# Kernel tuning notes

Measured on AMD Instinct MI355X. Metric: run time of the kernel, lower is better.

Reference implementation:

```python
import jax, jax.numpy as jnp
import numpy as np

B, T, D, E, H, K = 4, 1024, 1024, 8, 4096, 2
N = B * T
EPS_LN = 1e-5
EPS_W = 1e-8
BAL_W = 0.01


def setup_inputs() -> dict:
    key = jax.random.key(0)
    ks = jax.random.split(key, 5)
    sc = 0.02
    return {
        "x": jax.random.normal(ks[0], (B, T, D), jnp.float32),
        "ln_gamma": jnp.ones((D,), jnp.float32),
        "ln_beta": jnp.zeros((D,), jnp.float32),
        "gate_w": jax.random.normal(ks[1], (D, E), jnp.float32) * sc,
        "w1": jax.random.normal(ks[2], (E, D, H), jnp.float32) * sc,
        "b1": jnp.zeros((E, H), jnp.float32),
        "w2": jax.random.normal(ks[3], (E, H, D), jnp.float32) * sc,
        "b2": jnp.zeros((E, D), jnp.float32),
    }


def reference(x, ln_gamma, ln_beta, gate_w, w1, b1, w2, b2):
    # LayerNorm (pre-norm), residual kept on raw x
    mu = jnp.mean(x, axis=-1, keepdims=True)
    var = jnp.var(x, axis=-1, keepdims=True)
    xn = (x - mu) * jax.lax.rsqrt(var + EPS_LN) * ln_gamma + ln_beta

    xf = xn.reshape(N, D)

    # Router (oscillator_state=None path): token gate only, k = top_k
    logits = xf @ gate_w                         # (N, E)
    router_probs = jax.nn.softmax(logits, axis=-1)
    top_w, top_i = jax.lax.top_k(router_probs, K)  # (N, K)
    top_w = top_w / (jnp.sum(top_w, axis=-1, keepdims=True) + EPS_W)

    # Dense per-token gate matrix: gates[n, e] = sum of top-k weights routed to e
    gates = jnp.zeros((N, E), xf.dtype).at[jnp.arange(N)[:, None], top_i].add(top_w)

    # Per-expert FFN (computed densely for all tokens, combined by sparse gates)
    h = jax.nn.gelu(jnp.einsum("nd,edh->enh", xf, w1) + b1[:, None, :], approximate=False)
    expert_out = jnp.einsum("enh,ehd->end", h, w2) + b2[:, None, :]  # (E, N, D)
    moe = jnp.einsum("ne,end->nd", gates, expert_out)

    output = x + moe.reshape(B, T, D)

    # Load-balance auxiliary loss
    counts = jnp.zeros((E,), xf.dtype).at[top_i.reshape(-1)].add(1.0)
    fraction = counts / N
    balance_loss = BAL_W * E * jnp.sum(fraction * jnp.mean(router_probs, axis=0))

    return output, balance_loss, router_probs
```

## Files before the change

kernel.cpp:

```cpp
#include <hip/hip_runtime.h>
#include <hip/hip_bf16.h>
#include <math.h>

#define DI   1024
#define EI   8
#define HI   4096
#define NI   4096

typedef __bf16 bf16x8 __attribute__((ext_vector_type(8)));
typedef float  f32x4  __attribute__((ext_vector_type(4)));

__device__ __forceinline__ unsigned short f2bf(float f) {
  union { float f; unsigned u; } c; c.f = f;
  unsigned r = c.u + 0x7FFF + ((c.u >> 16) & 1);
  return (unsigned short)(r >> 16);
}

__device__ __forceinline__ void async16(const void* g, void* l) {
  __builtin_amdgcn_global_load_lds(
      (const __attribute__((address_space(1))) void*)g,
      (__attribute__((address_space(3))) void*)l, 16, 0, 0);
}

__global__ __launch_bounds__(256) void ln_router_k(
    const float* __restrict__ x, const float* __restrict__ gamma,
    const float* __restrict__ beta, const float* __restrict__ gw,
    unsigned short* __restrict__ xnbf, float* __restrict__ probs_out,
    int* __restrict__ pairs, float2* __restrict__ gates2)
{
  const int t = threadIdx.x, lane = t & 63, wid = t >> 6;
  const int n = blockIdx.x * 4 + wid;

  const float4* xr = (const float4*)(x + (size_t)n * DI);
  float4 v[4];
  #pragma unroll
  for (int j = 0; j < 4; j++) v[j] = xr[lane * 4 + j];

  float s = 0.f, q = 0.f;
  #pragma unroll
  for (int j = 0; j < 4; j++) {
    s += v[j].x + v[j].y + v[j].z + v[j].w;
    q += v[j].x * v[j].x + v[j].y * v[j].y + v[j].z * v[j].z + v[j].w * v[j].w;
  }
  #pragma unroll
  for (int off = 1; off < 64; off <<= 1) {
    s += __shfl_xor(s, off);
    q += __shfl_xor(q, off);
  }
  const float mu = s * (1.0f / DI);
  const float rs = rsqrtf(q * (1.0f / DI) - mu * mu + 1e-5f);

  const float4* gr = (const float4*)gamma;
  const float4* br = (const float4*)beta;
  float xl[16];
  #pragma unroll
  for (int j = 0; j < 4; j++) {
    const float4 g4 = gr[lane * 4 + j];
    const float4 b4 = br[lane * 4 + j];
    xl[4 * j + 0] = (v[j].x - mu) * rs * g4.x + b4.x;
    xl[4 * j + 1] = (v[j].y - mu) * rs * g4.y + b4.y;
    xl[4 * j + 2] = (v[j].z - mu) * rs * g4.z + b4.z;
    xl[4 * j + 3] = (v[j].w - mu) * rs * g4.w + b4.w;
  }
  unsigned u[8];
  #pragma unroll
  for (int j = 0; j < 8; j++)
    u[j] = (unsigned)f2bf(xl[2 * j]) | ((unsigned)f2bf(xl[2 * j + 1]) << 16);
  uint4* dst = (uint4*)(xnbf + (size_t)n * DI + lane * 16);
  uint4 d0; d0.x = u[0]; d0.y = u[1]; d0.z = u[2]; d0.w = u[3];
  uint4 d1; d1.x = u[4]; d1.y = u[5]; d1.z = u[6]; d1.w = u[7];
  dst[0] = d0; dst[1] = d1;

  float p[8];
  #pragma unroll
  for (int e = 0; e < 8; e++) p[e] = 0.f;
  #pragma unroll
  for (int j = 0; j < 16; j++) {
    const float4* grow = (const float4*)(gw + (size_t)(lane * 16 + j) * EI);
    const float4 ga = grow[0], gb = grow[1];
    const float xv = xl[j];
    p[0] += xv * ga.x; p[1] += xv * ga.y; p[2] += xv * ga.z; p[3] += xv * ga.w;
    p[4] += xv * gb.x; p[5] += xv * gb.y; p[6] += xv * gb.z; p[7] += xv * gb.w;
  }
  #pragma unroll
  for (int e = 0; e < 8; e++)
    #pragma unroll
    for (int off = 1; off < 64; off <<= 1) p[e] += __shfl_xor(p[e], off);

  if (lane == 0) {
    float pm = -1e30f;
    #pragma unroll
    for (int e = 0; e < 8; e++) pm = fmaxf(pm, p[e]);
    float pr[8], ps = 0.f;
    #pragma unroll
    for (int e = 0; e < 8; e++) { pr[e] = expf(p[e] - pm); ps += pr[e]; }
    const float inv = 1.0f / ps;
    #pragma unroll
    for (int e = 0; e < 8; e++) {
      pr[e] *= inv;
      probs_out[(size_t)n * EI + e] = pr[e];
    }
    int i0 = 0; float m0 = pr[0];
    #pragma unroll
    for (int e = 1; e < 8; e++) if (pr[e] > m0) { m0 = pr[e]; i0 = e; }
    int i1 = -1; float m1 = -1e30f;
    #pragma unroll
    for (int e = 0; e < 8; e++) if (e != i0 && pr[e] > m1) { m1 = pr[e]; i1 = e; }
    const float ssum = m0 + m1 + 1e-8f;
    pairs[n] = i0 | (i1 << 8);
    float2 g2; g2.x = m0 / ssum; g2.y = m1 / ssum;
    gates2[n] = g2;
  }
}

__global__ __launch_bounds__(1024) void build_lists_k(
    const int* __restrict__ pairs, const float2* __restrict__ gates2,
    const float* __restrict__ probs, int* __restrict__ counts,
    int* __restrict__ offs, int* __restrict__ tok_list,
    float* __restrict__ gate_list, int2* __restrict__ ipos,
    float* __restrict__ out_bal)
{
  __shared__ int cnt[8];
  __shared__ int cur[8];
  __shared__ float wps[16][8];
  __shared__ float ps[8];
  const int t = threadIdx.x, lane = t & 63, wid = t >> 6;
  if (t < 8) cnt[t] = 0;
  __syncthreads();

  float acc[8];
  #pragma unroll
  for (int e = 0; e < 8; e++) acc[e] = 0.f;
  for (int n = t; n < NI; n += 1024) {
    const int pr = pairs[n];
    atomicAdd(&cnt[pr & 255], 1);
    atomicAdd(&cnt[pr >> 8], 1);
    const float4* prow = (const float4*)(probs + (size_t)n * EI);
    const float4 a = prow[0], b = prow[1];
    acc[0] += a.x; acc[1] += a.y; acc[2] += a.z; acc[3] += a.w;
    acc[4] += b.x; acc[5] += b.y; acc[6] += b.z; acc[7] += b.w;
  }
  #pragma unroll
  for (int e = 0; e < 8; e++)
    #pragma unroll
    for (int off = 1; off < 64; off <<= 1) acc[e] += __shfl_xor(acc[e], off);
  if (lane == 0)
    #pragma unroll
    for (int e = 0; e < 8; e++) wps[wid][e] = acc[e];
  __syncthreads();
  if (t < 8) {
    float sm = 0.f;
    for (int w = 0; w < 16; w++) sm += wps[w][t];
    ps[t] = sm;
  }
  __syncthreads();
  if (t == 0) {
    int off = 0; float bl = 0.f;
    for (int e = 0; e < 8; e++) {
      offs[e] = off; cur[e] = off; counts[e] = cnt[e];
      bl += (float)cnt[e] * ps[e];
      off += cnt[e];
    }
    *out_bal = 0.01f * 8.0f * bl / ((float)NI * (float)NI);
  }
  __syncthreads();
  for (int n = t; n < NI; n += 1024) {
    const int pr = pairs[n];
    const float2 g = gates2[n];
    const int p0 = atomicAdd(&cur[pr & 255], 1);
    tok_list[p0] = n; gate_list[p0] = g.x;
    const int p1 = atomicAdd(&cur[pr >> 8], 1);
    tok_list[p1] = n; gate_list[p1] = g.y;
    int2 ip; ip.x = p0; ip.y = p1;
    ipos[n] = ip;
  }
}

__global__ __launch_bounds__(256) void transpose_cvt_k(
    const float* __restrict__ in, unsigned short* __restrict__ out, int R, int C)
{
  __shared__ float tile[64][65];
  const size_t eoff = (size_t)blockIdx.z * (size_t)R * (size_t)C;
  const int c0 = blockIdx.x * 64, r0 = blockIdx.y * 64;
  const int t = threadIdx.x;
  {
    const int col = (t & 15) * 4;
    #pragma unroll
    for (int ii = 0; ii < 4; ii++) {
      const int row = (t >> 4) + ii * 16;
      const float4 v = *(const float4*)(in + eoff + (size_t)(r0 + row) * C + c0 + col);
      tile[row][col + 0] = v.x; tile[row][col + 1] = v.y;
      tile[row][col + 2] = v.z; tile[row][col + 3] = v.w;
    }
  }
  __syncthreads();
  {
    const int grp = t & 7;
    #pragma unroll
    for (int jj = 0; jj < 2; jj++) {
      const int orow = (t >> 3) + jj * 32;
      unsigned short vs[8];
      #pragma unroll
      for (int u = 0; u < 8; u++) vs[u] = f2bf(tile[grp * 8 + u][orow]);
      uint4 pk;
      pk.x = (unsigned)vs[0] | ((unsigned)vs[1] << 16);
      pk.y = (unsigned)vs[2] | ((unsigned)vs[3] << 16);
      pk.z = (unsigned)vs[4] | ((unsigned)vs[5] << 16);
      pk.w = (unsigned)vs[6] | ((unsigned)vs[7] << 16);
      *(uint4*)(out + eoff + (size_t)(c0 + orow) * R + r0 + grp * 8) = pk;
    }
  }
}

__global__ __launch_bounds__(256) void copy_x_k(const float* __restrict__ x, float* __restrict__ out)
{
  const size_t i = (size_t)blockIdx.x * 256 + threadIdx.x;
  ((float4*)out)[i] = ((const float4*)x)[i];
}

__global__ __launch_bounds__(256) void ffn1_k(
    const unsigned short* __restrict__ xnbf, const unsigned short* __restrict__ w1t,
    const float* __restrict__ b1, unsigned short* __restrict__ hbuf,
    const int* __restrict__ tok_list, const int* __restrict__ counts,
    const int* __restrict__ offsets)
{
  const int e = blockIdx.z;
  const int cnt = counts[e];
  const int mt = blockIdx.y;
  if (mt * 128 >= cnt) return;
  const int n0 = blockIdx.x * 128;
  const int t = threadIdx.x, lane = t & 63, w = t >> 6;
  const int wm = w & 1, wn = w >> 1;
  __shared__ __align__(16) unsigned short As[128 * 64];
  __shared__ __align__(16) unsigned short Bs[128 * 64];

  const int sub = lane >> 3;
  const int kc = (((lane & 7) ^ sub) * 8);
  const int eoff = offsets[e];
  const unsigned short* baseA[4];
  const unsigned short* baseB[4];
  #pragma unroll
  for (int r = 0; r < 4; r++) {
    int row = (w << 5) + r * 8 + sub;
    int idx = mt * 128 + row; if (idx > cnt - 1) idx = cnt - 1;
    int tok = tok_list[eoff + idx];
    baseA[r] = xnbf + (size_t)tok * DI + kc;
    baseB[r] = w1t + (size_t)e * HI * DI + (size_t)(n0 + row) * DI + kc;
  }

  f32x4 acc[4][4];
  const f32x4 zz = {0.f, 0.f, 0.f, 0.f};
  #pragma unroll
  for (int i = 0; i < 4; i++)
    #pragma unroll
    for (int j = 0; j < 4; j++) acc[i][j] = zz;

  const int mrow = (wm << 6) + (lane & 15);
  const int nrow = (wn << 6) + (lane & 15);
  const int ksw[2] = { (((lane >> 4) ^ (lane & 7)) * 8),
                       ((((lane >> 4) + 4) ^ (lane & 7)) * 8) };

  for (int k0 = 0; k0 < DI; k0 += 64) {
    __syncthreads();
    #pragma unroll
    for (int r = 0; r < 4; r++) {
      async16(baseA[r] + k0, &As[((w << 5) + r * 8) * 64]);
      async16(baseB[r] + k0, &Bs[((w << 5) + r * 8) * 64]);
    }
    __syncthreads();
    #pragma unroll
    for (int kk = 0; kk < 2; kk++) {
      const int ko = ksw[kk];
      bf16x8 af[4], bfr[4];
      #pragma unroll
      for (int mi = 0; mi < 4; mi++)
        af[mi] = *(const bf16x8*)&As[(mrow + mi * 16) * 64 + ko];
      #pragma unroll
      for (int ni = 0; ni < 4; ni++)
        bfr[ni] = *(const bf16x8*)&Bs[(nrow + ni * 16) * 64 + ko];
      #pragma unroll
      for (int mi = 0; mi < 4; mi++)
        #pragma unroll
        for (int ni = 0; ni < 4; ni++)
          acc[mi][ni] = __builtin_amdgcn_mfma_f32_16x16x32_bf16(af[mi], bfr[ni], acc[mi][ni], 0, 0, 0);
    }
  }

  const int hb = eoff + mt * 128;
  #pragma unroll
  for (int ni = 0; ni < 4; ni++) {
    const int col = n0 + (wn << 6) + ni * 16 + (lane & 15);
    const float bias = b1[e * HI + col];
    #pragma unroll
    for (int mi = 0; mi < 4; mi++) {
      #pragma unroll
      for (int rg = 0; rg < 4; rg++) {
        const int rowl = (wm << 6) + mi * 16 + ((lane >> 4) << 2) + rg;
        if (mt * 128 + rowl < cnt) {
          float vv = acc[mi][ni][rg] + bias;
          vv = 0.5f * vv * (1.0f + erff(vv * 0.70710678118f));
          hbuf[(size_t)(hb + rowl) * HI + col] = f2bf(vv);
        }
      }
    }
  }
}

__global__ __launch_bounds__(256) void ffn2_k(
    const unsigned short* __restrict__ hbuf, const unsigned short* __restrict__ w2t,
    const float* __restrict__ b2, float* __restrict__ out,
    const int* __restrict__ tok_list, const float* __restrict__ gate_list,
    const int* __restrict__ counts, const int* __restrict__ offsets,
    float* __restrict__ eo)
{
  const int e = blockIdx.z;
  const int cnt = counts[e];
  const int mt = blockIdx.y;
  if (mt * 128 >= cnt) return;
  const int n0 = blockIdx.x * 128;
  const int t = threadIdx.x, lane = t & 63, w = t >> 6;
  const int wm = w & 1, wn = w >> 1;
  __shared__ __align__(16) unsigned short As[128 * 64];
  __shared__ __align__(16) unsigned short Bs[128 * 64];

  const int sub = lane >> 3;
  const int kc = (((lane & 7) ^ sub) * 8);
  const int eoff = offsets[e];
  const int hb = eoff + mt * 128;
  const unsigned short* baseA[4];
  const unsigned short* baseB[4];
  #pragma unroll
  for (int r = 0; r < 4; r++) {
    int row = (w << 5) + r * 8 + sub;
    baseA[r] = hbuf + (size_t)(hb + row) * HI + kc;
    baseB[r] = w2t + (size_t)e * DI * HI + (size_t)(n0 + row) * HI + kc;
  }

  f32x4 acc[4][4];
  const f32x4 zz = {0.f, 0.f, 0.f, 0.f};
  #pragma unroll
  for (int i = 0; i < 4; i++)
    #pragma unroll
    for (int j = 0; j < 4; j++) acc[i][j] = zz;

  const int mrow = (wm << 6) + (lane & 15);
  const int nrow = (wn << 6) + (lane & 15);
  const int ksw[2] = { (((lane >> 4) ^ (lane & 7)) * 8),
                       ((((lane >> 4) + 4) ^ (lane & 7)) * 8) };

  for (int k0 = 0; k0 < HI; k0 += 64) {
    __syncthreads();
    #pragma unroll
    for (int r = 0; r < 4; r++) {
      async16(baseA[r] + k0, &As[((w << 5) + r * 8) * 64]);
      async16(baseB[r] + k0, &Bs[((w << 5) + r * 8) * 64]);
    }
    __syncthreads();
    #pragma unroll
    for (int kk = 0; kk < 2; kk++) {
      const int ko = ksw[kk];
      bf16x8 af[4], bfr[4];
      #pragma unroll
      for (int mi = 0; mi < 4; mi++)
        af[mi] = *(const bf16x8*)&As[(mrow + mi * 16) * 64 + ko];
      #pragma unroll
      for (int ni = 0; ni < 4; ni++)
        bfr[ni] = *(const bf16x8*)&Bs[(nrow + ni * 16) * 64 + ko];
      #pragma unroll
      for (int mi = 0; mi < 4; mi++)
        #pragma unroll
        for (int ni = 0; ni < 4; ni++)
          acc[mi][ni] = __builtin_amdgcn_mfma_f32_16x16x32_bf16(af[mi], bfr[ni], acc[mi][ni], 0, 0, 0);
    }
  }

  float bias[4];
  #pragma unroll
  for (int ni = 0; ni < 4; ni++)
    bias[ni] = b2[e * DI + n0 + (wn << 6) + ni * 16 + (lane & 15)];

  if (eo) {
    #pragma unroll
    for (int mi = 0; mi < 4; mi++) {
      #pragma unroll
      for (int rg = 0; rg < 4; rg++) {
        const int rowl = (wm << 6) + mi * 16 + ((lane >> 4) << 2) + rg;
        const int gidx = mt * 128 + rowl;
        if (gidx < cnt) {
          float* erow = eo + (size_t)(hb + rowl) * DI;
          #pragma unroll
          for (int ni = 0; ni < 4; ni++) {
            const int col = n0 + (wn << 6) + ni * 16 + (lane & 15);
            erow[col] = acc[mi][ni][rg] + bias[ni];
          }
        }
      }
    }
  } else {
    #pragma unroll
    for (int mi = 0; mi < 4; mi++) {
      #pragma unroll
      for (int rg = 0; rg < 4; rg++) {
        const int rowl = (wm << 6) + mi * 16 + ((lane >> 4) << 2) + rg;
        const int gidx = mt * 128 + rowl;
        if (gidx < cnt) {
          const int tok = tok_list[eoff + gidx];
          const float gte = gate_list[eoff + gidx];
          float* orow = out + (size_t)tok * DI;
          #pragma unroll
          for (int ni = 0; ni < 4; ni++) {
            const int col = n0 + (wn << 6) + ni * 16 + (lane & 15);
            atomicAdd(orow + col, (acc[mi][ni][rg] + bias[ni]) * gte);
          }
        }
      }
    }
  }
}

__global__ __launch_bounds__(256) void combine_k(
    const float* __restrict__ x, const float* __restrict__ eo,
    const int2* __restrict__ ipos, const float2* __restrict__ gates2,
    float* __restrict__ out)
{
  const int n = blockIdx.x, t = threadIdx.x;
  const int2 pp = ipos[n];
  const float2 gg = gates2[n];
  const float4 a = ((const float4*)(x  + (size_t)n    * DI))[t];
  const float4 b = ((const float4*)(eo + (size_t)pp.x * DI))[t];
  const float4 c = ((const float4*)(eo + (size_t)pp.y * DI))[t];
  float4 r;
  r.x = a.x + gg.x * b.x + gg.y * c.x;
  r.y = a.y + gg.x * b.y + gg.y * c.y;
  r.z = a.z + gg.x * b.z + gg.y * c.z;
  r.w = a.w + gg.x * b.w + gg.y * c.w;
  ((float4*)(out + (size_t)n * DI))[t] = r;
}

extern "C" void kernel_launch(void* const* d_in, const int* in_sizes, int n_in,
                              void* d_out, int out_size, void* d_ws, size_t ws_size,
                              hipStream_t stream)
{
  const float* x   = (const float*)d_in[0];
  const float* gam = (const float*)d_in[1];
  const float* bet = (const float*)d_in[2];
  const float* gw  = (const float*)d_in[3];
  const float* w1  = (const float*)d_in[4];
  const float* b1  = (const float*)d_in[5];
  const float* w2  = (const float*)d_in[6];
  const float* b2  = (const float*)d_in[7];
  float* out = (float*)d_out;

  char* ws = (char*)d_ws;
  int*    counts = (int*)(ws + 0);
  int*    offs   = (int*)(ws + 64);
  int*    pairs  = (int*)(ws + 1024);
  float2* gates2 = (float2*)(ws + 20480);
  int*    tok    = (int*)(ws + 57344);
  float*  gate   = (float*)(ws + 90112);
  int2*   ipos   = (int2*)(ws + 122880);
  unsigned short* xnbf = (unsigned short*)(ws + 262656);
  unsigned short* wt   = (unsigned short*)(ws + 8651264);
  unsigned short* hbuf = (unsigned short*)(ws + 75760128);
  const bool use_eo = (ws_size >= 177472000ull);
  float* eo = use_eo ? (float*)(ws + 143917568) : (float*)nullptr;

  float* bal_out   = out + (size_t)NI * DI;
  float* probs_out = bal_out + 1;

  ln_router_k<<<NI / 4, 256, 0, stream>>>(x, gam, bet, gw, xnbf, probs_out, pairs, gates2);
  build_lists_k<<<1, 1024, 0, stream>>>(pairs, gates2, probs_out, counts, offs, tok, gate, ipos, bal_out);
  transpose_cvt_k<<<dim3(HI / 64, DI / 64, EI), 256, 0, stream>>>(w1, wt, DI, HI);
  if (!use_eo)
    copy_x_k<<<(NI * DI / 4) / 256, 256, 0, stream>>>(x, out);
  ffn1_k<<<dim3(HI / 128, NI / 128, EI), 256, 0, stream>>>(xnbf, wt, b1, hbuf, tok, counts, offs);
  transpose_cvt_k<<<dim3(DI / 64, HI / 64, EI), 256, 0, stream>>>(w2, wt, HI, DI);
  ffn2_k<<<dim3(DI / 128, NI / 128, EI), 256, 0, stream>>>(hbuf, wt, b2, out, tok, gate, counts, offs, eo);
  if (use_eo)
    combine_k<<<NI, 256, 0, stream>>>(x, eo, ipos, gates2, out);
}
```

Measured before the change: 661.5 us.

## Double-buffer LDS tiles in expert GEMMs and use fast polynomial GELU

Both expert FFN GEMM kernels now use two LDS buffers per operand. The async global-to-LDS load for the next K-tile is issued before the MFMA work on the current tile, which cuts one barrier per iteration and overlaps memory latency with compute. The exact erff-based GELU in FFN1 is replaced by an Abramowitz-Stegun polynomial erf approximation using rcp and exp. In exchange, LDS use per block doubles to 64 KB, which may lower occupancy, and GELU accuracy drops slightly.

```diff
diff --git a/kernel.cpp b/kernel.cpp
--- a/kernel.cpp
+++ b/kernel.cpp
@@ -21,6 +21,41 @@
       (const __attribute__((address_space(1))) void*)g,
       (__attribute__((address_space(3))) void*)l, 16, 0, 0);
 }
+
+__device__ __forceinline__ float gelu_fast(float v) {
+  const float a = fabsf(v) * 0.70710678118f;
+  const float t = __builtin_amdgcn_rcpf(fmaf(0.3275911f, a, 1.0f));
+  float p = fmaf(1.061405429f, t, -1.453152027f);
+  p = fmaf(p, t, 1.421413741f);
+  p = fmaf(p, t, -0.284496736f);
+  p = fmaf(p, t, 0.254829592f);
+  p *= t;
+  const float ex = __expf(-a * a);
+  float er = fmaf(-p, ex, 1.0f);
+  er = copysignf(er, v);
+  return 0.5f * v * (1.0f + er);
+}
+
+#define MFMA_TILE(ASP, BSP)                                              \
+  {                                                                      \
+    _Pragma("unroll")                                                    \
+    for (int kk = 0; kk < 2; kk++) {                                     \
+      const int ko = ksw[kk];                                            \
+      bf16x8 af[4], bfr[4];                                              \
+      _Pragma("unroll")                                                  \
+      for (int mi = 0; mi < 4; mi++)                                     \
+        af[mi] = *(const bf16x8*)&(ASP)[(mrow + mi * 16) * 64 + ko];     \
+      _Pragma("unroll")                                                  \
+      for (int ni = 0; ni < 4; ni++)                                     \
+        bfr[ni] = *(const bf16x8*)&(BSP)[(nrow + ni * 16) * 64 + ko];    \
+      _Pragma("unroll")                                                  \
+      for (int mi = 0; mi < 4; mi++)                                     \
+        _Pragma("unroll")                                                \
+        for (int ni = 0; ni < 4; ni++)                                   \
+          acc[mi][ni] = __builtin_amdgcn_mfma_f32_16x16x32_bf16(         \
+              af[mi], bfr[ni], acc[mi][ni], 0, 0, 0);                    \
+    }                                                                    \
+  }
 
 __global__ __launch_bounds__(256) void ln_router_k(
     const float* __restrict__ x, const float* __restrict__ gamma,
@@ -231,8 +266,8 @@
   const int n0 = blockIdx.x * 128;
   const int t = threadIdx.x, lane = t & 63, w = t >> 6;
   const int wm = w & 1, wn = w >> 1;
-  __shared__ __align__(16) unsigned short As[128 * 64];
-  __shared__ __align__(16) unsigned short Bs[128 * 64];
+  __shared__ __align__(16) unsigned short As[2][128 * 64];
+  __shared__ __align__(16) unsigned short Bs[2][128 * 64];
 
   const int sub = lane >> 3;
   const int kc = (((lane & 7) ^ sub) * 8);
@@ -260,31 +295,27 @@
   const int ksw[2] = { (((lane >> 4) ^ (lane & 7)) * 8),
                        ((((lane >> 4) + 4) ^ (lane & 7)) * 8) };
 
-  for (int k0 = 0; k0 < DI; k0 += 64) {
+  #pragma unroll
+  for (int r = 0; r < 4; r++) {
+    async16(baseA[r], &As[0][((w << 5) + r * 8) * 64]);
+    async16(baseB[r], &Bs[0][((w << 5) + r * 8) * 64]);
+  }
+  __syncthreads();
+
+  #pragma unroll 2
+  for (int ti = 1; ti < DI / 64; ti++) {
+    const int nb = ti & 1;
+    const int cb = nb ^ 1;
+    const int k0 = ti * 64;
+    #pragma unroll
+    for (int r = 0; r < 4; r++) {
+      async16(baseA[r] + k0, &As[nb][((w << 5) + r * 8) * 64]);
+      async16(baseB[r] + k0, &Bs[nb][((w << 5) + r * 8) * 64]);
+    }
+    MFMA_TILE(As[cb], Bs[cb]);
     __syncthreads();
-    #pragma unroll
-    for (int r = 0; r < 4; r++) {
-      async16(baseA[r] + k0, &As[((w << 5) + r * 8) * 64]);
-      async16(baseB[r] + k0, &Bs[((w << 5) + r * 8) * 64]);
-    }
-    __syncthreads();
-    #pragma unroll
-    for (int kk = 0; kk < 2; kk++) {
-      const int ko = ksw[kk];
-      bf16x8 af[4], bfr[4];
-      #pragma unroll
-      for (int mi = 0; mi < 4; mi++)
-        af[mi] = *(const bf16x8*)&As[(mrow + mi * 16) * 64 + ko];
-      #pragma unroll
-      for (int ni = 0; ni < 4; ni++)
-        bfr[ni] = *(const bf16x8*)&Bs[(nrow + ni * 16) * 64 + ko];
-      #pragma unroll
-      for (int mi = 0; mi < 4; mi++)
-        #pragma unroll
-        for (int ni = 0; ni < 4; ni++)
-          acc[mi][ni] = __builtin_amdgcn_mfma_f32_16x16x32_bf16(af[mi], bfr[ni], acc[mi][ni], 0, 0, 0);
-    }
-  }
+  }
+  MFMA_TILE(As[(DI / 64 - 1) & 1], Bs[(DI / 64 - 1) & 1]);
 
   const int hb = eoff + mt * 128;
   #pragma unroll
@@ -297,8 +328,7 @@
       for (int rg = 0; rg < 4; rg++) {
         const int rowl = (wm << 6) + mi * 16 + ((lane >> 4) << 2) + rg;
         if (mt * 128 + rowl < cnt) {
-          float vv = acc[mi][ni][rg] + bias;
-          vv = 0.5f * vv * (1.0f + erff(vv * 0.70710678118f));
+          const float vv = gelu_fast(acc[mi][ni][rg] + bias);
           hbuf[(size_t)(hb + rowl) * HI + col] = f2bf(vv);
         }
       }
@@ -320,8 +350,8 @@
   const int n0 = blockIdx.x * 128;
   const int t = threadIdx.x, lane = t & 63, w = t >> 6;
   const int wm = w & 1, wn = w >> 1;
-  __shared__ __align__(16) unsigned short As[128 * 64];
-  __shared__ __align__(16) unsigned short Bs[128 * 64];
+  __shared__ __align__(16) unsigned short As[2][128 * 64];
+  __shared__ __align__(16) unsigned short Bs[2][128 * 64];
 
   const int sub = lane >> 3;
   const int kc = (((lane & 7) ^ sub) * 8);
@@ -348,31 +378,27 @@
   const int ksw[2] = { (((lane >> 4) ^ (lane & 7)) * 8),
                        ((((lane >> 4) + 4) ^ (lane & 7)) * 8) };
 
-  for (int k0 = 0; k0 < HI; k0 += 64) {
+  #pragma unroll
+  for (int r = 0; r < 4; r++) {
+    async16(baseA[r], &As[0][((w << 5) + r * 8) * 64]);
+    async16(baseB[r], &Bs[0][((w << 5) + r * 8) * 64]);
+  }
+  __syncthreads();
+
+  #pragma unroll 2
+  for (int ti = 1; ti < HI / 64; ti++) {
+    const int nb = ti & 1;
+    const int cb = nb ^ 1;
+    const int k0 = ti * 64;
+    #pragma unroll
+    for (int r = 0; r < 4; r++) {
+      async16(baseA[r] + k0, &As[nb][((w << 5) + r * 8) * 64]);
+      async16(baseB[r] + k0, &Bs[nb][((w << 5) + r * 8) * 64]);
+    }
+    MFMA_TILE(As[cb], Bs[cb]);
     __syncthreads();
-    #pragma unroll
-    for (int r = 0; r < 4; r++) {
-      async16(baseA[r] + k0, &As[((w << 5) + r * 8) * 64]);
-      async16(baseB[r] + k0, &Bs[((w << 5) + r * 8) * 64]);
-    }
-    __syncthreads();
-    #pragma unroll
-    for (int kk = 0; kk < 2; kk++) {
-      const int ko = ksw[kk];
-      bf16x8 af[4], bfr[4];
-      #pragma unroll
-      for (int mi = 0; mi < 4; mi++)
-        af[mi] = *(const bf16x8*)&As[(mrow + mi * 16) * 64 + ko];
-      #pragma unroll
-      for (int ni = 0; ni < 4; ni++)
-        bfr[ni] = *(const bf16x8*)&Bs[(nrow + ni * 16) * 64 + ko];
-      #pragma unroll
-      for (int mi = 0; mi < 4; mi++)
-        #pragma unroll
-        for (int ni = 0; ni < 4; ni++)
-          acc[mi][ni] = __builtin_amdgcn_mfma_f32_16x16x32_bf16(af[mi], bfr[ni], acc[mi][ni], 0, 0, 0);
-    }
-  }
+  }
+  MFMA_TILE(As[(HI / 64 - 1) & 1], Bs[(HI / 64 - 1) & 1]);
 
   float bias[4];
   #pragma unroll
```

Measured after the change: 675.1 us. 2.1% more time.
